# Kernel optimization log

Measured on AMD Instinct MI355X. Metric: run time of the kernel, lower is better.

## Reference

```python
import jax, jax.numpy as jnp
import numpy as np

B = 128; DIM_IN = 3; MAX_CYCLE = 50; NODES = 18
T = MAX_CYCLE * NODES          # cycle_size = 900
F1, F2 = 32, 64                # stgcn_filters
NCLS = 3
N = B * T                      # nodes seen by GATv2 = 115200
E = 12 * N                     # edges (avg degree 12)
EPS = 1e-5


def setup_inputs() -> dict:
    key = jax.random.key(0)
    keys = iter(jax.random.split(key, 48))
    def p(shape, scale=0.05):
        return jax.random.normal(next(keys), shape, jnp.float32) * scale
    inp = {}
    inp["x"] = jax.random.normal(next(keys), (B, DIM_IN, T), jnp.float32)
    inp["edge_index"] = jax.random.randint(next(keys), (2, E), 0, N)
    def block(pfx, cin, c):
        inp[pfx + "_tc1_w"] = p((c, cin, 5)); inp[pfx + "_tc1_b"] = p((c,))
        inp[pfx + "_wl"] = p((c, c)); inp[pfx + "_bl"] = p((c,))
        inp[pfx + "_wr"] = p((c, c)); inp[pfx + "_br"] = p((c,))
        inp[pfx + "_att"] = p((c,)); inp[pfx + "_gbias"] = p((c,))
        inp[pfx + "_bn_g"] = jnp.ones((c,), jnp.float32)
        inp[pfx + "_bn_b"] = jnp.zeros((c,), jnp.float32)
        inp[pfx + "_tc2_w"] = p((c, c, 5)); inp[pfx + "_tc2_b"] = p((c,))
    block("b1", DIM_IN, F1)
    block("b2", F1, F2)
    inp["fc1_w"] = p((128, T * F2), 0.01); inp["fc1_b"] = p((128,))
    inp["hbn1_g"] = jnp.ones((128,), jnp.float32); inp["hbn1_b"] = jnp.zeros((128,), jnp.float32)
    inp["fc2_w"] = p((64, 128)); inp["fc2_b"] = p((64,))
    inp["hbn2_g"] = jnp.ones((64,), jnp.float32); inp["hbn2_b"] = jnp.zeros((64,), jnp.float32)
    inp["fc3_w"] = p((NCLS, 64)); inp["fc3_b"] = p((NCLS,))
    return inp


def _conv1d_same(x, w, b):
    # x: [B, Cin, T], w: [Cout, Cin, 5], 'same' padding (pad 2/2)
    y = jax.lax.conv_general_dilated(x, w, (1,), [(2, 2)],
                                     dimension_numbers=("NCH", "OIH", "NCH"))
    return y + b[None, :, None]


def _bn(h, g, b):
    # BatchNorm1d on [N, C] with batch statistics
    m = h.mean(0)
    v = h.var(0)
    return (h - m) * jax.lax.rsqrt(v + EPS) * g + b


def _gatv2(h, src, dst, wl, bl, wr, br, att, gbias):
    # PyG GATv2Conv, heads=1, negative_slope=0.2, self loops already in src/dst
    xl = h @ wl.T + bl            # source transform, also the message
    xr = h @ wr.T + br            # target transform
    e = jnp.dot(jax.nn.leaky_relu(xl[src] + xr[dst], 0.2), att)  # [E]
    m = jax.ops.segment_max(e, dst, num_segments=N)
    ex = jnp.exp(e - m[dst])
    s = jax.ops.segment_sum(ex, dst, num_segments=N)
    alpha = ex / s[dst]
    out = jax.ops.segment_sum(alpha[:, None] * xl[src], dst, num_segments=N)
    return out + gbias


def _block(x, src, dst, tc1_w, tc1_b, wl, bl, wr, br, att, gbias, bn_g, bn_b, tc2_w, tc2_b):
    x = jax.nn.relu(_conv1d_same(x, tc1_w, tc1_b))      # [B, C, T]
    C = tc1_w.shape[0]
    h = x.reshape(T * B, C)                             # torch .view(T*B, C) (raw row-major)
    h = jax.nn.relu(_gatv2(h, src, dst, wl, bl, wr, br, att, gbias))
    h = _bn(h, bn_g, bn_b)
    h = h.reshape(B, C, T)                              # torch .view(B, C, T)
    return jax.nn.relu(_conv1d_same(h, tc2_w, tc2_b))


def reference(x, edge_index,
              b1_tc1_w, b1_tc1_b, b1_wl, b1_bl, b1_wr, b1_br, b1_att, b1_gbias,
              b1_bn_g, b1_bn_b, b1_tc2_w, b1_tc2_b,
              b2_tc1_w, b2_tc1_b, b2_wl, b2_bl, b2_wr, b2_br, b2_att, b2_gbias,
              b2_bn_g, b2_bn_b, b2_tc2_w, b2_tc2_b,
              fc1_w, fc1_b, hbn1_g, hbn1_b, fc2_w, fc2_b, hbn2_g, hbn2_b, fc3_w, fc3_b):
    sl = jnp.arange(N, dtype=edge_index.dtype)          # PyG add_self_loops=True
    src = jnp.concatenate([edge_index[0], sl])
    dst = jnp.concatenate([edge_index[1], sl])
    h = _block(x, src, dst, b1_tc1_w, b1_tc1_b, b1_wl, b1_bl, b1_wr, b1_br,
               b1_att, b1_gbias, b1_bn_g, b1_bn_b, b1_tc2_w, b1_tc2_b)
    h = jax.nn.relu(h)                                  # extra relu on non-final block (dropout off)
    h = _block(h, src, dst, b2_tc1_w, b2_tc1_b, b2_wl, b2_bl, b2_wr, b2_br,
               b2_att, b2_gbias, b2_bn_g, b2_bn_b, b2_tc2_w, b2_tc2_b)
    h = h.reshape(B, F2 * T)
    h = jax.nn.relu(h @ fc1_w.T + fc1_b)
    h = _bn(h, hbn1_g, hbn1_b)
    h = jax.nn.relu(h @ fc2_w.T + fc2_b)
    h = _bn(h, hbn2_g, hbn2_b)
    logits = h @ fc3_w.T + fc3_b
    return (jax.nn.sigmoid(logits), logits)
```

## Files before the change

kernel.cpp:

```cpp
#include <hip/hip_runtime.h>
#include <hip/hip_bf16.h>

typedef __hip_bfloat16 bf16;
typedef __attribute__((ext_vector_type(8))) short s16x8;
typedef __attribute__((ext_vector_type(4))) float f32x4;
#define DEV static __device__ __forceinline__

DEV float b2f(bf16 v){ return __bfloat162float(v); }
DEV bf16  f2b(float v){ return __float2bfloat16(v); }
DEV int   is_f32(const void* gones){ return ((const unsigned int*)gones)[0] == 0x3F800000u ? 1 : 0; }
DEV float ldin(const void* p, int f32, int i){
    return f32 ? ((const float*)p)[i] : __bfloat162float(((const bf16*)p)[i]);
}
DEV void unpk(unsigned u, float& a, float& b){
    a = __uint_as_float(u << 16);
    b = __uint_as_float(u & 0xffff0000u);
}
DEV float lrelu(float t){ return fmaxf(t, 0.f) + 0.2f * fminf(t, 0.f); }
DEV unsigned short bfu(float v){ bf16 h = f2b(v); return *(unsigned short*)&h; }

constexpr int Bb  = 128;
constexpr int Tt  = 900;
constexpr int Nn  = Bb * Tt;
constexpr int Ee  = 12 * Nn;
constexpr int CAP = 48;
constexpr int NBK  = 256;
constexpr int NPB  = Nn / NBK;
constexpr int BCAP = 8192;
constexpr int WROWS = 96 + 1024 + 2048 + 4096;
constexpr int WTOT  = WROWS * 5;
constexpr int WBF   = 5120 + 10240 + 20480;
constexpr int WXT   = 2*32*32 + 64 + 2*64*64 + 128;

__global__ __launch_bounds__(256) void k_wprep(const void* wa, const void* wb_, const void* wc,
    const void* wd,
    const void* b1wl, const void* b1bl, const void* b1wr, const void* b1br,
    const void* b2wl, const void* b2bl, const void* b2wr, const void* b2br,
    const void* gones, float* __restrict__ wp, bf16* __restrict__ wbf,
    float* __restrict__ wx, int* __restrict__ gcur){
    const int f32 = is_f32(gones);
    if (blockIdx.x == 0 && threadIdx.x < NBK) gcur[threadIdx.x] = 0;
    int e = blockIdx.x * 256 + threadIdx.x;
    if (e < WTOT){
        int r = e / 5, k = e - r * 5;
        const void* src; int rb;
        if (r < 96)      { src = wa; rb = 0; }
        else if (r < 1120){ src = wb_; rb = 96; }
        else if (r < 3168){ src = wc; rb = 1120; }
        else             { src = wd; rb = 3168; }
        wp[r * 8 + k] = ldin(src, f32, (r - rb) * 5 + k);
    } else if (e < WTOT + WBF){
        int e2 = e - WTOT;
        const void* src; int kk, r;
        if (e2 < 5120)      { kk = e2 >> 10; r = e2 & 1023; src = wb_; }
        else if (e2 < 15360){ int e3 = e2 - 5120;  kk = e3 >> 11; r = e3 & 2047; src = wc; }
        else                { int e3 = e2 - 15360; kk = e3 >> 12; r = e3 & 4095; src = wd; }
        wbf[e2] = f2b(ldin(src, f32, r * 5 + kk));
    } else if (e < WTOT + WBF + WXT){
        int e3 = e - WTOT - WBF;
        float v;
        if      (e3 < 1024){ int t = e3;         int c = t >> 5, f = t & 31; v = ldin(b1wl, f32, f * 32 + c); }
        else if (e3 < 2048){ int t = e3 - 1024;  int c = t >> 5, f = t & 31; v = ldin(b1wr, f32, f * 32 + c); }
        else if (e3 < 2080)  v = ldin(b1bl, f32, e3 - 2048);
        else if (e3 < 2112)  v = ldin(b1br, f32, e3 - 2080);
        else if (e3 < 6208){ int t = e3 - 2112;  int c = t >> 6, f = t & 63; v = ldin(b2wl, f32, f * 64 + c); }
        else if (e3 < 10304){int t = e3 - 6208;  int c = t >> 6, f = t & 63; v = ldin(b2wr, f32, f * 64 + c); }
        else if (e3 < 10368) v = ldin(b2bl, f32, e3 - 10304);
        else                 v = ldin(b2br, f32, e3 - 10368);
        wx[e3] = v;
    }
}

__global__ __launch_bounds__(256) void k_bucket(const int* __restrict__ ei,
                                                int* __restrict__ gcur, int2* __restrict__ bkt){
    constexpr int TILE = 4096;
    const int base = blockIdx.x * TILE;
    const int tid = threadIdx.x;
    __shared__ int cnt[NBK];
    __shared__ int gbase[NBK];
    cnt[tid] = 0;
    __syncthreads();
    int es[16], er[16], eb[16], rk[16];
    #pragma unroll
    for (int k = 0; k < 16; ++k){
        int idx = base + k * 256 + tid;
        if (idx < Ee){
            es[k] = ei[idx];
            int d = ei[Ee + idx];
            eb[k] = d / NPB;
            er[k] = d - eb[k] * NPB;
            rk[k] = atomicAdd(&cnt[eb[k]], 1);
        } else eb[k] = -1;
    }
    __syncthreads();
    {
        int c = cnt[tid];
        gbase[tid] = (c > 0) ? atomicAdd(&gcur[tid], c) : 0;
    }
    __syncthreads();
    #pragma unroll
    for (int k = 0; k < 16; ++k){
        if (eb[k] >= 0){
            int slot = gbase[eb[k]] + rk[k];
            if (slot < BCAP)
                bkt[(size_t)eb[k] * BCAP + slot] = make_int2(er[k], es[k]);
        }
    }
}

__global__ __launch_bounds__(256) void k_csr2(const int2* __restrict__ bkt, const int* __restrict__ gcur,
                                              int* __restrict__ csr, int* __restrict__ cnt){
    const int b = blockIdx.x;
    const int n0 = b * NPB;
    __shared__ int lcnt[NPB];
    for (int i = threadIdx.x; i < NPB; i += 256) lcnt[i] = 0;
    __syncthreads();
    const int tot = min(gcur[b], BCAP);
    for (int i = threadIdx.x; i < tot; i += 256){
        int2 e = bkt[(size_t)b * BCAP + i];
        int p = atomicAdd(&lcnt[e.x], 1);
        if (p < CAP) csr[(size_t)(n0 + e.x) * CAP + p] = e.y;
    }
    __syncthreads();
    for (int i = threadIdx.x; i < NPB; i += 256) cnt[n0 + i] = lcnt[i];
}

template<bool EXT, int CIN, int COUT, bool BN>
__global__ __launch_bounds__(256) void k_conv(const void* __restrict__ x,
    const float* __restrict__ wp, int wbase,
    const void* __restrict__ bias, const float* __restrict__ scale, const float* __restrict__ shift,
    const void* __restrict__ gones, float* __restrict__ y)
{
    const int f32 = is_f32(gones);
    __shared__ alignas(16) float xs[CIN][132];
    const int b = blockIdx.x >> 3, t0 = (blockIdx.x & 7) * 128;
    const int tid = threadIdx.x;
    for (int i = tid; i < CIN * 132; i += 256){
        int ci = i / 132, tt = i % 132;
        int gt = t0 + tt - 2;
        float v = 0.f;
        if (gt >= 0 && gt < Tt){
            int idx = (b * CIN + ci) * Tt + gt;
            v = EXT ? ldin(x, f32, idx) : ((const float*)x)[idx];
            if (BN){
                int f = (ci * (Tt % CIN) + gt) % CIN;
                v = v * scale[f] + shift[f];
            }
        }
        xs[ci][tt] = v;
    }
    __syncthreads();
    constexpr int HALF = COUT / 2;
    constexpr int NT   = 256 / HALF;
    constexpr int NW   = 128 / (NT * 4);
    const int cop = tid / NT;
    const int tch = tid % NT;
    const int co = cop, co2 = cop + HALF;
    float acc[NW][2][4];
    #pragma unroll
    for (int iw = 0; iw < NW; ++iw)
        #pragma unroll
        for (int h = 0; h < 2; ++h)
            #pragma unroll
            for (int j = 0; j < 4; ++j) acc[iw][h][j] = 0.f;

    const float* w0p = wp + (size_t)(wbase + co  * CIN) * 8;
    const float* w1p = wp + (size_t)(wbase + co2 * CIN) * 8;
    float4 na = *(const float4*)w0p; float na4 = w0p[4];
    float4 nb = *(const float4*)w1p; float nb4 = w1p[4];
    for (int ci = 0; ci < CIN; ++ci){
        const float w0[5] = {na.x, na.y, na.z, na.w, na4};
        const float w1[5] = {nb.x, nb.y, nb.z, nb.w, nb4};
        if (ci + 1 < CIN){
            const float* p0 = w0p + (size_t)(ci + 1) * 8;
            const float* p1 = w1p + (size_t)(ci + 1) * 8;
            na = *(const float4*)p0; na4 = p0[4];
            nb = *(const float4*)p1; nb4 = p1[4];
        }
        #pragma unroll
        for (int iw = 0; iw < NW; ++iw){
            const int tl = tch * 4 + iw * NT * 4;
            float4 a  = *(const float4*)&xs[ci][tl];
            float4 bq = *(const float4*)&xs[ci][tl + 4];
            float xw[8] = {a.x,a.y,a.z,a.w,bq.x,bq.y,bq.z,bq.w};
            #pragma unroll
            for (int k = 0; k < 5; ++k)
                #pragma unroll
                for (int j = 0; j < 4; ++j){
                    acc[iw][0][j] = fmaf(xw[j + k], w0[k], acc[iw][0][j]);
                    acc[iw][1][j] = fmaf(xw[j + k], w1[k], acc[iw][1][j]);
                }
        }
    }
    const float bv0 = ldin(bias, f32, co), bv1 = ldin(bias, f32, co2);
    #pragma unroll
    for (int iw = 0; iw < NW; ++iw){
        const int t = t0 + tch * 4 + iw * NT * 4;
        if (t < Tt){
            float4 o0, o1;
            o0.x = fmaxf(acc[iw][0][0] + bv0, 0.f); o0.y = fmaxf(acc[iw][0][1] + bv0, 0.f);
            o0.z = fmaxf(acc[iw][0][2] + bv0, 0.f); o0.w = fmaxf(acc[iw][0][3] + bv0, 0.f);
            o1.x = fmaxf(acc[iw][1][0] + bv1, 0.f); o1.y = fmaxf(acc[iw][1][1] + bv1, 0.f);
            o1.z = fmaxf(acc[iw][1][2] + bv1, 0.f); o1.w = fmaxf(acc[iw][1][3] + bv1, 0.f);
            *(float4*)&y[(b * COUT + co ) * Tt + t] = o0;
            *(float4*)&y[(b * COUT + co2) * Tt + t] = o1;
        }
    }
}

template<int CIN, int COUT, bool BN>
__global__ __launch_bounds__(256) void k_convM(const float* __restrict__ x, const bf16* __restrict__ wbf,
    int wbase,
    const void* __restrict__ bias, const float* __restrict__ scale, const float* __restrict__ shift,
    const void* __restrict__ gones, float* __restrict__ y)
{
    const int f32 = is_f32(gones);
    constexpr int STR = CIN + 8;
    constexpr int CI2 = CIN / 2;
    __shared__ alignas(16) float smem[COUT * 132];
    unsigned short* xsT = (unsigned short*)smem;
    const int b = blockIdx.x >> 3, t0 = (blockIdx.x & 7) * 128;
    const int tid = threadIdx.x;
    for (int i = tid; i < CI2 * 128; i += 256){
        int ci2 = i >> 7, tt = i & 127;
        int gt = t0 + tt - 2;
        int ci = ci2 * 2;
        unsigned pack = 0;
        if (gt >= 0 && gt < Tt){
            float v0 = x[(b * CIN + ci) * Tt + gt];
            float v1 = x[(b * CIN + ci + 1) * Tt + gt];
            if (BN){
                int fa = (4 * ci + gt) & (CIN - 1), fb = (4 * ci + 4 + gt) & (CIN - 1);
                v0 = v0 * scale[fa] + shift[fa];
                v1 = v1 * scale[fb] + shift[fb];
            }
            pack = (unsigned)bfu(v0) | ((unsigned)bfu(v1) << 16);
        }
        *(unsigned*)&xsT[tt * STR + ci] = pack;
    }
    if (tid < CI2 * 4){
        int ci2 = tid >> 2, tt = 128 + (tid & 3);
        int gt = t0 + tt - 2;
        int ci = ci2 * 2;
        unsigned pack = 0;
        if (gt < Tt){
            float v0 = x[(b * CIN + ci) * Tt + gt];
            float v1 = x[(b * CIN + ci + 1) * Tt + gt];
            if (BN){
                int fa = (4 * ci + gt) & (CIN - 1), fb = (4 * ci + 4 + gt) & (CIN - 1);
                v0 = v0 * scale[fa] + shift[fa];
                v1 = v1 * scale[fb] + shift[fb];
            }
            pack = (unsigned)bfu(v0) | ((unsigned)bfu(v1) << 16);
        }
        *(unsigned*)&xsT[tt * STR + ci] = pack;
    }
    __syncthreads();
    const int lane = tid & 63, wid = tid >> 6;
    const int l15 = lane & 15, quad = lane >> 4;
    constexpr int MT  = COUT / 16;
    constexpr int NTP = 2 * MT;
    const int mt  = (MT == 4) ? wid : (wid & 1);
    const int ntb = (MT == 4) ? 0 : (wid >> 1) * NTP;
    const int co0 = mt * 16;
    f32x4 acc[NTP];
    #pragma unroll
    for (int nt = 0; nt < NTP; ++nt){ f32x4 z = {0.f, 0.f, 0.f, 0.f}; acc[nt] = z; }
    for (int kk = 0; kk < 5; ++kk){
        #pragma unroll
        for (int kb = 0; kb < CIN / 32; ++kb){
            s16x8 a = *(const s16x8*)&wbf[wbase + kk * (COUT * CIN) + (co0 + l15) * CIN + kb * 32 + quad * 8];
            #pragma unroll
            for (int nt = 0; nt < NTP; ++nt){
                s16x8 bf = *(const s16x8*)&xsT[((ntb + nt) * 16 + l15 + kk) * STR + kb * 32 + quad * 8];
                acc[nt] = __builtin_amdgcn_mfma_f32_16x16x32_bf16(a, bf, acc[nt], 0, 0, 0);
            }
        }
    }
    __syncthreads();
    #pragma unroll
    for (int nt = 0; nt < NTP; ++nt)
        #pragma unroll
        for (int r = 0; r < 4; ++r)
            smem[(co0 + quad * 4 + r) * 132 + (ntb + nt) * 16 + l15] = acc[nt][r];
    __syncthreads();
    for (int i = tid; i < COUT * 32; i += 256){
        int co = i >> 5, c4 = (i & 31) << 2;
        int t = t0 + c4;
        if (t < Tt){
            float4 o = *(float4*)&smem[co * 132 + c4];
            float bb = ldin(bias, f32, co);
            o.x = fmaxf(o.x + bb, 0.f); o.y = fmaxf(o.y + bb, 0.f);
            o.z = fmaxf(o.z + bb, 0.f); o.w = fmaxf(o.w + bb, 0.f);
            float* dst = &y[(b * COUT + co) * Tt + t];
            if (t + 3 < Tt) *(float4*)dst = o;
            else {
                float ov[4] = {o.x, o.y, o.z, o.w};
                for (int j = 0; j < 4 && t + j < Tt; ++j) dst[j] = ov[j];
            }
        }
    }
}

template<int C>
__global__ __launch_bounds__(256) void k_xlxr(const float* __restrict__ h,
    const float* __restrict__ wx, int wxoff,
    unsigned short* __restrict__ xlh, float* __restrict__ xr)
{
    constexpr int NB = 4096 / C;
    constexpr int HS = NB + 4;
    __shared__ alignas(16) float hT[C][HS];
    __shared__ alignas(16) float wlS[C * C];
    __shared__ alignas(16) float wrS[C * C];
    const int tid = threadIdx.x;
    const int n0 = blockIdx.x * NB;
    for (int i = tid; i < NB * C; i += 256){
        int n = i & (NB - 1), c = i / NB;
        hT[c][n] = h[(size_t)(n0 + n) * C + c];
    }
    const float* wl = wx + wxoff;
    const float* wr = wl + C * C;
    for (int i = tid; i < C * C; i += 256){
        wlS[i] = wl[i];
        wrS[i] = wr[i];
    }
    __syncthreads();
    const float* bl = wr + C * C;
    const float* br = bl + C;
    constexpr int FG = C / 4;
    const int fg = tid % FG, ng = tid / FG;
    const int nloc = ng * 4, floc = fg * 4;
    float blv[4], brv[4];
    #pragma unroll
    for (int j = 0; j < 4; ++j){ blv[j] = bl[floc + j]; brv[j] = br[floc + j]; }
    float accL[4][4], accR[4][4];
    #pragma unroll
    for (int i = 0; i < 4; ++i)
        #pragma unroll
        for (int j = 0; j < 4; ++j){ accL[i][j] = 0.f; accR[i][j] = 0.f; }
    #pragma unroll 4
    for (int c = 0; c < C; ++c){
        float4 hv = *(const float4*)&hT[c][nloc];
        float4 lv = *(const float4*)&wlS[c * C + floc];
        float4 rv = *(const float4*)&wrS[c * C + floc];
        float ha[4] = {hv.x,hv.y,hv.z,hv.w};
        float la[4] = {lv.x,lv.y,lv.z,lv.w};
        float ra[4] = {rv.x,rv.y,rv.z,rv.w};
        #pragma unroll
        for (int i = 0; i < 4; ++i)
            #pragma unroll
            for (int j = 0; j < 4; ++j){
                accL[i][j] = fmaf(ha[i], la[j], accL[i][j]);
                accR[i][j] = fmaf(ha[i], ra[j], accR[i][j]);
            }
    }
    #pragma unroll
    for (int i = 0; i < 4; ++i){
        size_t n = n0 + nloc + i;
        bf16 hb[4];
        hb[0] = f2b(accL[i][0] + blv[0]); hb[1] = f2b(accL[i][1] + blv[1]);
        hb[2] = f2b(accL[i][2] + blv[2]); hb[3] = f2b(accL[i][3] + blv[3]);
        *(ushort4*)&xlh[n * C + floc] = *(ushort4*)hb;
        float4 r;
        r.x = accR[i][0] + brv[0]; r.y = accR[i][1] + brv[1];
        r.z = accR[i][2] + brv[2]; r.w = accR[i][3] + brv[3];
        *(float4*)&xr[n * C + floc] = r;
    }
}

template<int L> DEV float rsumL(float v){
    #pragma unroll
    for (int s = L / 2; s > 0; s >>= 1) v += __shfl_xor(v, s, 64);
    return v;
}

template<int C, int FPL>
__global__ __launch_bounds__(256) void k_gat(const unsigned short* __restrict__ xlh,
    const float* __restrict__ xr,
    const int* __restrict__ csr, const int* __restrict__ cnt,
    const void* __restrict__ att, const void* __restrict__ gbias,
    const void* __restrict__ gones, float* __restrict__ out)
{
    const int f32 = is_f32(gones);
    constexpr int L   = C / FPL;
    constexpr int NPW = 64 / L;
    const int lane = threadIdx.x & 63, wid = threadIdx.x >> 6;
    const int sub = lane / L, fp = lane % L;
    const int node = (blockIdx.x * 4 + wid) * NPW + sub;
    const int f0 = FPL * fp;
    float xrv[FPL], a1v[FPL], a2v[FPL];
    if constexpr (FPL == 4){
        float4 t = *(const float4*)&xr[(size_t)node * C + f0];
        xrv[0] = t.x; xrv[1] = t.y; xrv[2] = t.z; xrv[3] = t.w;
    } else {
        float2 t = *(const float2*)&xr[(size_t)node * C + f0];
        xrv[0] = t.x; xrv[1] = t.y;
    }
    #pragma unroll
    for (int i = 0; i < FPL; ++i){
        float a = ldin(att, f32, f0 + i);
        a1v[i] = 0.6f * a;
        a2v[i] = 0.4f * a;
    }
    const int deg = min(cnt[node], CAP);
    int degu = deg;
    degu = max(degu, __shfl_xor(degu, 32, 64));
    degu = max(degu, __shfl_xor(degu, 16, 64));

    auto loadv = [&](int s, float (&v)[FPL]){
        if constexpr (FPL == 4){
            uint2 u = *(const uint2*)&xlh[(size_t)s * C + f0];
            unpk(u.x, v[0], v[1]); unpk(u.y, v[2], v[3]);
        } else {
            unsigned u = *(const unsigned*)&xlh[(size_t)s * C + f0];
            unpk(u, v[0], v[1]);
        }
    };
    auto score = [&](const float (&v)[FPL]){
        float l = 0.f;
        #pragma unroll
        for (int i = 0; i < FPL; ++i){
            float t = v[i] + xrv[i];
            l = fmaf(a1v[i], t, l);
            l = fmaf(a2v[i], fabsf(t), l);
        }
        return rsumL<L>(l);
    };

    float ssum, acc[FPL];
    {
        float v[FPL];
        loadv(node, v);
        float w = __expf(score(v));
        ssum = w;
        #pragma unroll
        for (int i = 0; i < FPL; ++i) acc[i] = w * v[i];
    }
    for (int j = 0; j < degu; j += 8){
        const int* crow = &csr[(size_t)node * CAP + j];
        int4 sa = *(const int4*)crow;
        int4 sb = *(const int4*)(crow + 4);
        int ss[8] = {sa.x, sa.y, sa.z, sa.w, sb.x, sb.y, sb.z, sb.w};
        bool av[8];
        #pragma unroll
        for (int q = 0; q < 8; ++q){
            av[q] = (j + q < deg);
            if (!av[q]) ss[q] = node;
        }
        float v[8][FPL];
        #pragma unroll
        for (int q = 0; q < 8; ++q) loadv(ss[q], v[q]);
        float e[8];
        #pragma unroll
        for (int q = 0; q < 8; ++q) e[q] = score(v[q]);
        #pragma unroll
        for (int q = 0; q < 8; ++q){
            float w = av[q] ? __expf(e[q]) : 0.f;
            ssum += w;
            #pragma unroll
            for (int i = 0; i < FPL; ++i) acc[i] = fmaf(w, v[q][i], acc[i]);
        }
    }
    float inv = 1.f / ssum;
    if constexpr (FPL == 4){
        float4 o;
        o.x = fmaxf(fmaf(acc[0], inv, ldin(gbias, f32, f0)),     0.f);
        o.y = fmaxf(fmaf(acc[1], inv, ldin(gbias, f32, f0 + 1)), 0.f);
        o.z = fmaxf(fmaf(acc[2], inv, ldin(gbias, f32, f0 + 2)), 0.f);
        o.w = fmaxf(fmaf(acc[3], inv, ldin(gbias, f32, f0 + 3)), 0.f);
        *(float4*)&out[(size_t)node * C + f0] = o;
    } else {
        float2 o;
        o.x = fmaxf(fmaf(acc[0], inv, ldin(gbias, f32, f0)),     0.f);
        o.y = fmaxf(fmaf(acc[1], inv, ldin(gbias, f32, f0 + 1)), 0.f);
        *(float2*)&out[(size_t)node * C + f0] = o;
    }
}

template<int C>
__global__ __launch_bounds__(256) void k_bnstat1(const float* __restrict__ h, double* __restrict__ part){
    const int tid = threadIdx.x;
    double s1 = 0.0, s2 = 0.0;
    const int total = Nn * C;
    for (int idx = blockIdx.x * 256 + tid; idx < total; idx += 65536){
        float v = h[idx];
        s1 += v; s2 += (double)v * v;
    }
    __shared__ double r1[256], r2[256];
    r1[tid] = s1; r2[tid] = s2;
    __syncthreads();
    if (tid < C){
        double a = 0.0, b = 0.0;
        #pragma unroll
        for (int q = 0; q < 256 / C; ++q){ a += r1[tid + q * C]; b += r2[tid + q * C]; }
        part[blockIdx.x * 2 * C + tid]     = a;
        part[blockIdx.x * 2 * C + C + tid] = b;
    }
}

template<int C>
__global__ void k_bnstat2(const double* __restrict__ part, const void* __restrict__ g,
                          const void* __restrict__ b, const void* __restrict__ gones,
                          float* __restrict__ scale, float* __restrict__ shift){
    const int f32 = is_f32(gones);
    const int f = threadIdx.x;
    double s1 = 0.0, s2 = 0.0;
    for (int s = 0; s < 256; ++s){ s1 += part[s * 2 * C + f]; s2 += part[s * 2 * C + C + f]; }
    double mean = s1 / (double)Nn;
    double var  = s2 / (double)Nn - mean * mean;
    float sc = (float)((double)ldin(g, f32, f) / sqrt(var + 1e-5));
    float sh = ldin(b, f32, f) - (float)mean * sc;
    scale[f] = sc; shift[f] = sh;
}

__global__ __launch_bounds__(256) void k_fc1(const float* __restrict__ h, const void* __restrict__ w1,
                                             const void* __restrict__ gones, float* __restrict__ part){
    const int f32 = is_f32(gones);
    __shared__ alignas(16) float AT[32][136];
    __shared__ alignas(16) float BT[32][136];
    const int tid = threadIdx.x;
    const int blk = blockIdx.x;
    const int k0 = blk * 128;
    const int bg = tid >> 4, jg = tid & 15;
    const int row = tid >> 5, kk = tid & 31;
    float ar[16], br[16];
    #pragma unroll
    for (int q = 0; q < 16; ++q){
        int idx = (row + q * 8) * 57600 + k0 + kk;
        ar[q] = h[idx];
        br[q] = ldin(w1, f32, idx);
    }
    float acc[8][8];
    #pragma unroll
    for (int i = 0; i < 8; ++i)
        #pragma unroll
        for (int j = 0; j < 8; ++j) acc[i][j] = 0.f;
    for (int ch = 0; ch < 4; ++ch){
        __syncthreads();
        #pragma unroll
        for (int q = 0; q < 16; ++q){
            AT[kk][row + q * 8] = ar[q];
            BT[kk][row + q * 8] = br[q];
        }
        __syncthreads();
        if (ch < 3){
            const int kb = k0 + (ch + 1) * 32;
            #pragma unroll
            for (int q = 0; q < 16; ++q){
                int idx = (row + q * 8) * 57600 + kb + kk;
                ar[q] = h[idx];
                br[q] = ldin(w1, f32, idx);
            }
        }
        for (int k2 = 0; k2 < 32; ++k2){
            float4 a0 = *(const float4*)&AT[k2][bg * 8];
            float4 a1 = *(const float4*)&AT[k2][bg * 8 + 4];
            float4 c0 = *(const float4*)&BT[k2][jg * 8];
            float4 c1 = *(const float4*)&BT[k2][jg * 8 + 4];
            float av[8] = {a0.x,a0.y,a0.z,a0.w,a1.x,a1.y,a1.z,a1.w};
            float bv[8] = {c0.x,c0.y,c0.z,c0.w,c1.x,c1.y,c1.z,c1.w};
            #pragma unroll
            for (int i = 0; i < 8; ++i)
                #pragma unroll
                for (int j = 0; j < 8; ++j) acc[i][j] = fmaf(av[i], bv[j], acc[i][j]);
        }
    }
    #pragma unroll
    for (int i = 0; i < 8; ++i){
        int bb = bg * 8 + i;
        #pragma unroll
        for (int q = 0; q < 2; ++q){
            float4 o;
            o.x = acc[i][q*4+0]; o.y = acc[i][q*4+1]; o.z = acc[i][q*4+2]; o.w = acc[i][q*4+3];
            *(float4*)&part[blk * 16384 + bb * 128 + jg * 8 + q * 4] = o;
        }
    }
}

__global__ void k_fc1red1(const float* __restrict__ part, float* __restrict__ pr2){
    const int y = blockIdx.x >> 6;
    const int o = (blockIdx.x & 63) * 256 + threadIdx.x;
    const int sb0 = y * 57;
    const int sb1 = min(sb0 + 57, 450);
    float s = 0.f;
    for (int sb = sb0; sb < sb1; ++sb) s += part[(size_t)sb * 16384 + o];
    pr2[(size_t)y * 16384 + o] = s;
}

__global__ void k_fc1red2(const float* __restrict__ pr2, const void* __restrict__ bias,
                          const void* __restrict__ gones, float* __restrict__ out1){
    const int f32 = is_f32(gones);
    const int o = blockIdx.x * 256 + threadIdx.x;
    float s = ldin(bias, f32, o & 127);
    #pragma unroll
    for (int y = 0; y < 8; ++y) s += pr2[(size_t)y * 16384 + o];
    out1[o] = fmaxf(s, 0.f);
}

__global__ void k_hstat(const float* __restrict__ out1, const void* __restrict__ g1,
                        const void* __restrict__ b1, const void* __restrict__ gones,
                        float* __restrict__ sc, float* __restrict__ sh){
    const int f32 = is_f32(gones);
    const int f = threadIdx.x;
    double s1 = 0.0, s2 = 0.0;
    for (int r = 0; r < 128; ++r){ float v = out1[r * 128 + f]; s1 += v; s2 += (double)v * v; }
    double mean = s1 / 128.0, var = s2 / 128.0 - mean * mean;
    float s = (float)((double)ldin(g1, f32, f) / sqrt(var + 1e-5));
    sc[f] = s;
    sh[f] = ldin(b1, f32, f) - (float)mean * s;
}

__global__ __launch_bounds__(256) void k_fc2(const float* __restrict__ out1,
    const float* __restrict__ sc, const float* __restrict__ sh,
    const void* __restrict__ w2, const void* __restrict__ fb2,
    const void* __restrict__ gones, float* __restrict__ f2)
{
    const int f32 = is_f32(gones);
    __shared__ alignas(16) float hs[4 * 128];
    __shared__ alignas(16) float w2s[64 * 132];
    const int tid = threadIdx.x;
    const int b0 = blockIdx.x * 4;
    for (int i = tid; i < 512; i += 256){
        int f = i & 127;
        hs[i] = out1[b0 * 128 + i] * sc[f] + sh[f];
    }
    for (int i = tid; i < 8192; i += 256)
        w2s[(i >> 7) * 132 + (i & 127)] = ldin(w2, f32, i);
    __syncthreads();
    const int b = tid >> 6, o = tid & 63;
    float acc = ldin(fb2, f32, o);
    const float* hp = &hs[b * 128];
    const float* wq = &w2s[o * 132];
    #pragma unroll
    for (int k = 0; k < 128; k += 4){
        float4 hv = *(const float4*)&hp[k];
        float4 wv = *(const float4*)&wq[k];
        acc = fmaf(hv.x, wv.x, acc); acc = fmaf(hv.y, wv.y, acc);
        acc = fmaf(hv.z, wv.z, acc); acc = fmaf(hv.w, wv.w, acc);
    }
    f2[(b0 + b) * 64 + o] = fmaxf(acc, 0.f);
}

__global__ __launch_bounds__(256) void k_head2(const float* __restrict__ f2,
    const void* g2, const void* b2v, const void* w3, const void* fb3,
    const void* gones, void* __restrict__ out)
{
    const int f32 = is_f32(gones);
    __shared__ float fs[8192];
    __shared__ float sc2[64], sh2[64];
    const int tid = threadIdx.x;
    for (int i = tid; i < 8192; i += 256) fs[i] = f2[i];
    __syncthreads();
    if (tid < 64){
        double s1 = 0.0, s2 = 0.0;
        for (int r = 0; r < 128; ++r){ float v = fs[r * 64 + tid]; s1 += v; s2 += (double)v * v; }
        double mean = s1 / 128.0, var = s2 / 128.0 - mean * mean;
        sc2[tid] = (float)((double)ldin(g2, f32, tid) / sqrt(var + 1e-5));
        sh2[tid] = ldin(b2v, f32, tid) - (float)mean * sc2[tid];
    }
    __syncthreads();
    if (tid < 128){
        float hv[64];
        for (int k = 0; k < 64; ++k) hv[k] = fs[tid * 64 + k] * sc2[k] + sh2[k];
        #pragma unroll
        for (int c = 0; c < 3; ++c){
            float acc = ldin(fb3, f32, c);
            for (int k = 0; k < 64; ++k) acc = fmaf(hv[k], ldin(w3, f32, c * 64 + k), acc);
            float sg = 1.f / (1.f + __expf(-acc));
            if (f32){
                ((float*)out)[384 + tid * 3 + c] = acc;
                ((float*)out)[tid * 3 + c] = sg;
            } else {
                ((bf16*)out)[384 + tid * 3 + c] = f2b(acc);
                ((bf16*)out)[tid * 3 + c] = f2b(sg);
            }
        }
    }
}

extern "C" void kernel_launch(void* const* d_in, const int* in_sizes, int n_in,
                              void* d_out, int out_size, void* d_ws, size_t ws_size,
                              hipStream_t stream)
{
    const void* x   = d_in[0];
    const int*  ei  = (const int*)d_in[1];
    const void* b1_tc1_w=d_in[2];  const void* b1_tc1_b=d_in[3];
    const void* b1_wl   =d_in[4];  const void* b1_bl   =d_in[5];
    const void* b1_wr   =d_in[6];  const void* b1_br   =d_in[7];
    const void* b1_att  =d_in[8];  const void* b1_gb   =d_in[9];
    const void* b1_g    =d_in[10]; const void* b1_bt   =d_in[11];
    const void* b1_tc2_w=d_in[12]; const void* b1_tc2_b=d_in[13];
    const void* b2_tc1_w=d_in[14]; const void* b2_tc1_b=d_in[15];
    const void* b2_wl   =d_in[16]; const void* b2_bl   =d_in[17];
    const void* b2_wr   =d_in[18]; const void* b2_br   =d_in[19];
    const void* b2_att  =d_in[20]; const void* b2_gb   =d_in[21];
    const void* b2_g    =d_in[22]; const void* b2_bt   =d_in[23];
    const void* b2_tc2_w=d_in[24]; const void* b2_tc2_b=d_in[25];
    const void* fc1_w=d_in[26]; const void* fc1_b=d_in[27];
    const void* hbn1_g=d_in[28]; const void* hbn1_b=d_in[29];
    const void* fc2_w=d_in[30]; const void* fc2_b=d_in[31];
    const void* hbn2_g=d_in[32]; const void* hbn2_b=d_in[33];
    const void* fc3_w=d_in[34]; const void* fc3_b=d_in[35];
    const void* gones = b1_g;

    float* ws = (float*)d_ws;
    const size_t NC = (size_t)Nn * 64;
    float* buf0 = ws;
    float* buf1 = ws + NC;
    float* buf2 = ws + 2 * NC;
    int*   csr  = (int*)(ws + 3 * NC);
    int*   cnt  = (int*)((char*)csr + (size_t)Nn * CAP * 4);
    double* bnp = (double*)((char*)cnt + (size_t)Nn * 4);
    float* scale = (float*)(bnp + 32768);
    float* shift = scale + 128;
    unsigned short* xlh = (unsigned short*)(shift + 128);
    int*   gcur = (int*)(xlh + (size_t)Nn * 64);
    float* wp   = (float*)(gcur + NBK);
    bf16*  wbf  = (bf16*)(wp + (size_t)WROWS * 8);
    float* wx   = (float*)(wbf + WBF);
    int2*  bkt  = (int2*)buf2;
    float* part = buf0;
    float* out1 = buf2;
    float* pr2  = buf2 + 16384;
    float* f2b_ = pr2 + 8 * 16384;
    float* hsc  = f2b_ + 8192;
    float* hsh  = hsc + 128;

    k_wprep <<<(WTOT + WBF + WXT + 255) / 256, 256, 0, stream>>>(
        b1_tc1_w, b1_tc2_w, b2_tc1_w, b2_tc2_w,
        b1_wl, b1_bl, b1_wr, b1_br, b2_wl, b2_bl, b2_wr, b2_br,
        gones, wp, wbf, wx, gcur);
    k_bucket<<<(Ee + 4095) / 4096, 256, 0, stream>>>(ei, gcur, bkt);
    k_csr2  <<<NBK, 256, 0, stream>>>(bkt, gcur, csr, cnt);

    k_conv<true, 3, 32, false><<<Bb * 8, 256, 0, stream>>>(x, wp, 0, b1_tc1_b, nullptr, nullptr, gones, buf0);
    k_xlxr<32><<<Nn / 128, 256, 0, stream>>>(buf0, wx, 0, xlh, buf1);
    k_gat<32, 2><<<Nn / 16, 256, 0, stream>>>(xlh, buf1, csr, cnt, b1_att, b1_gb, gones, buf2);
    k_bnstat1<32><<<256, 256, 0, stream>>>(buf2, bnp);
    k_bnstat2<32><<<1, 32, 0, stream>>>(bnp, b1_g, b1_bt, gones, scale, shift);
    k_convM<32, 32, true><<<Bb * 8, 256, 0, stream>>>(buf2, wbf, 0, b1_tc2_b, scale, shift, gones, buf0);

    k_convM<32, 64, false><<<Bb * 8, 256, 0, stream>>>(buf0, wbf, 5120, b2_tc1_b, nullptr, nullptr, gones, buf1);
    k_xlxr<64><<<Nn / 64, 256, 0, stream>>>(buf1, wx, 2112, xlh, buf2);
    k_gat<64, 4><<<Nn / 16, 256, 0, stream>>>(xlh, buf2, csr, cnt, b2_att, b2_gb, gones, buf0);
    k_bnstat1<64><<<256, 256, 0, stream>>>(buf0, bnp);
    k_bnstat2<64><<<1, 64, 0, stream>>>(bnp, b2_g, b2_bt, gones, scale, shift);
    k_convM<64, 64, true><<<Bb * 8, 256, 0, stream>>>(buf0, wbf, 15360, b2_tc2_b, scale, shift, gones, buf1);

    k_fc1<<<450, 256, 0, stream>>>(buf1, fc1_w, gones, part);
    k_fc1red1<<<512, 256, 0, stream>>>(part, pr2);
    k_fc1red2<<<64, 256, 0, stream>>>(pr2, fc1_b, gones, out1);
    k_hstat<<<1, 128, 0, stream>>>(out1, hbn1_g, hbn1_b, gones, hsc, hsh);
    k_fc2<<<32, 256, 0, stream>>>(out1, hsc, hsh, fc2_w, fc2_b, gones, f2b_);
    k_head2<<<1, 256, 0, stream>>>(f2b_, hbn2_g, hbn2_b, fc3_w, fc3_b, gones, d_out);
}
```

Before: 510.7 us.

## Fuse BatchNorm statistics into GATv2 aggregation kernel via atomic partials

Removes the separate k_bnstat1 pass by having each GAT block compute per-feature sum and sum-of-squares of its outputs. These are reduced with wave shuffles and shared memory, then atomically added into 256 double-precision partial slots. The partial buffer is zeroed inside the xlxr kernel's first block. It also switches layer-1 GAT to 4 features per lane (fewer lanes per node, more nodes per wave), which changes how the gather work is spread. The cost is extra shuffles, a block barrier and double atomics with contention per slot, but it saves a full re-read of the N×C activation.

```diff
diff --git a/kernel.cpp b/kernel.cpp
--- a/kernel.cpp
+++ b/kernel.cpp
@@ -305,7 +305,8 @@
 template<int C>
 __global__ __launch_bounds__(256) void k_xlxr(const float* __restrict__ h,
     const float* __restrict__ wx, int wxoff,
-    unsigned short* __restrict__ xlh, float* __restrict__ xr)
+    unsigned short* __restrict__ xlh, float* __restrict__ xr,
+    double* __restrict__ bnp)
 {
     constexpr int NB = 4096 / C;
     constexpr int HS = NB + 4;
@@ -314,6 +315,9 @@
     __shared__ alignas(16) float wrS[C * C];
     const int tid = threadIdx.x;
     const int n0 = blockIdx.x * NB;
+    if (blockIdx.x == 0){
+        for (int i = tid; i < 256 * 2 * C; i += 256) bnp[i] = 0.0;
+    }
     for (int i = tid; i < NB * C; i += 256){
         int n = i & (NB - 1), c = i / NB;
         hT[c][n] = h[(size_t)(n0 + n) * C + c];
@@ -379,7 +383,8 @@
     const float* __restrict__ xr,
     const int* __restrict__ csr, const int* __restrict__ cnt,
     const void* __restrict__ att, const void* __restrict__ gbias,
-    const void* __restrict__ gones, float* __restrict__ out)
+    const void* __restrict__ gones, float* __restrict__ out,
+    double* __restrict__ bnp)
 {
     const int f32 = is_f32(gones);
     constexpr int L   = C / FPL;
@@ -404,8 +409,8 @@
     }
     const int deg = min(cnt[node], CAP);
     int degu = deg;
-    degu = max(degu, __shfl_xor(degu, 32, 64));
-    degu = max(degu, __shfl_xor(degu, 16, 64));
+    #pragma unroll
+    for (int s = L; s < 64; s <<= 1) degu = max(degu, __shfl_xor(degu, s, 64));
 
     auto loadv = [&](int s, float (&v)[FPL]){
         if constexpr (FPL == 4){
@@ -462,39 +467,42 @@
         }
     }
     float inv = 1.f / ssum;
+    float ov[FPL];
+    #pragma unroll
+    for (int i = 0; i < FPL; ++i)
+        ov[i] = fmaxf(fmaf(acc[i], inv, ldin(gbias, f32, f0 + i)), 0.f);
     if constexpr (FPL == 4){
-        float4 o;
-        o.x = fmaxf(fmaf(acc[0], inv, ldin(gbias, f32, f0)),     0.f);
-        o.y = fmaxf(fmaf(acc[1], inv, ldin(gbias, f32, f0 + 1)), 0.f);
-        o.z = fmaxf(fmaf(acc[2], inv, ldin(gbias, f32, f0 + 2)), 0.f);
-        o.w = fmaxf(fmaf(acc[3], inv, ldin(gbias, f32, f0 + 3)), 0.f);
+        float4 o; o.x = ov[0]; o.y = ov[1]; o.z = ov[2]; o.w = ov[3];
         *(float4*)&out[(size_t)node * C + f0] = o;
     } else {
-        float2 o;
-        o.x = fmaxf(fmaf(acc[0], inv, ldin(gbias, f32, f0)),     0.f);
-        o.y = fmaxf(fmaf(acc[1], inv, ldin(gbias, f32, f0 + 1)), 0.f);
+        float2 o; o.x = ov[0]; o.y = ov[1];
         *(float2*)&out[(size_t)node * C + f0] = o;
     }
-}
-
-template<int C>
-__global__ __launch_bounds__(256) void k_bnstat1(const float* __restrict__ h, double* __restrict__ part){
+    float s1[FPL], s2[FPL];
+    #pragma unroll
+    for (int i = 0; i < FPL; ++i){ s1[i] = ov[i]; s2[i] = ov[i] * ov[i]; }
+    #pragma unroll
+    for (int s = L; s < 64; s <<= 1){
+        #pragma unroll
+        for (int i = 0; i < FPL; ++i){
+            s1[i] += __shfl_xor(s1[i], s, 64);
+            s2[i] += __shfl_xor(s2[i], s, 64);
+        }
+    }
+    __shared__ float wred[4][2][C];
+    if (sub == 0){
+        #pragma unroll
+        for (int i = 0; i < FPL; ++i){
+            wred[wid][0][f0 + i] = s1[i];
+            wred[wid][1][f0 + i] = s2[i];
+        }
+    }
+    __syncthreads();
     const int tid = threadIdx.x;
-    double s1 = 0.0, s2 = 0.0;
-    const int total = Nn * C;
-    for (int idx = blockIdx.x * 256 + tid; idx < total; idx += 65536){
-        float v = h[idx];
-        s1 += v; s2 += (double)v * v;
-    }
-    __shared__ double r1[256], r2[256];
-    r1[tid] = s1; r2[tid] = s2;
-    __syncthreads();
-    if (tid < C){
-        double a = 0.0, b = 0.0;
-        #pragma unroll
-        for (int q = 0; q < 256 / C; ++q){ a += r1[tid + q * C]; b += r2[tid + q * C]; }
-        part[blockIdx.x * 2 * C + tid]     = a;
-        part[blockIdx.x * 2 * C + C + tid] = b;
+    if (tid < 2 * C){
+        const int stat = tid >= C, f = tid - stat * C;
+        float t = (wred[0][stat][f] + wred[1][stat][f]) + (wred[2][stat][f] + wred[3][stat][f]);
+        atomicAdd(&bnp[(size_t)(blockIdx.x & 255) * 2 * C + stat * C + f], (double)t);
     }
 }
 
@@ -734,16 +742,14 @@
     k_csr2  <<<NBK, 256, 0, stream>>>(bkt, gcur, csr, cnt);
 
     k_conv<true, 3, 32, false><<<Bb * 8, 256, 0, stream>>>(x, wp, 0, b1_tc1_b, nullptr, nullptr, gones, buf0);
-    k_xlxr<32><<<Nn / 128, 256, 0, stream>>>(buf0, wx, 0, xlh, buf1);
-    k_gat<32, 2><<<Nn / 16, 256, 0, stream>>>(xlh, buf1, csr, cnt, b1_att, b1_gb, gones, buf2);
-    k_bnstat1<32><<<256, 256, 0, stream>>>(buf2, bnp);
+    k_xlxr<32><<<Nn / 128, 256, 0, stream>>>(buf0, wx, 0, xlh, buf1, bnp);
+    k_gat<32, 4><<<Nn / 32, 256, 0, stream>>>(xlh, buf1, csr, cnt, b1_att, b1_gb, gones, buf2, bnp);
     k_bnstat2<32><<<1, 32, 0, stream>>>(bnp, b1_g, b1_bt, gones, scale, shift);
     k_convM<32, 32, true><<<Bb * 8, 256, 0, stream>>>(buf2, wbf, 0, b1_tc2_b, scale, shift, gones, buf0);
 
     k_convM<32, 64, false><<<Bb * 8, 256, 0, stream>>>(buf0, wbf, 5120, b2_tc1_b, nullptr, nullptr, gones, buf1);
-    k_xlxr<64><<<Nn / 64, 256, 0, stream>>>(buf1, wx, 2112, xlh, buf2);
-    k_gat<64, 4><<<Nn / 16, 256, 0, stream>>>(xlh, buf2, csr, cnt, b2_att, b2_gb, gones, buf0);
-    k_bnstat1<64><<<256, 256, 0, stream>>>(buf0, bnp);
+    k_xlxr<64><<<Nn / 64, 256, 0, stream>>>(buf1, wx, 2112, xlh, buf2, bnp);
+    k_gat<64, 4><<<Nn / 16, 256, 0, stream>>>(xlh, buf2, csr, cnt, b2_att, b2_gb, gones, buf0, bnp);
     k_bnstat2<64><<<1, 64, 0, stream>>>(bnp, b2_g, b2_bt, gones, scale, shift);
     k_convM<64, 64, true><<<Bb * 8, 256, 0, stream>>>(buf0, wbf, 15360, b2_tc2_b, scale, shift, gones, buf1);
 
```

Result: faster. 480.9 us (-5.8%).
